# Optimization experiments

Hardware: AMD Instinct MI355X
Metric: run time of the kernel (lower is better)

Reference implementation:

```python
import jax, jax.numpy as jnp
import numpy as np

N_WIRES = 12
DEPTH = 4
IN_DIM = 256
BATCH = 4096


def _apply_rx(state, theta, wire, n):
    """Apply RX(theta) = [[cos(t/2), -i sin(t/2)], [-i sin(t/2), cos(t/2)]] on `wire`.
    state: (batch, 2^n) complex. theta: scalar or (batch,) float."""
    half = theta * 0.5
    c = jnp.reshape(jnp.cos(half), (-1, 1, 1))  # broadcasts for scalar or per-batch
    s = jnp.reshape(jnp.sin(half), (-1, 1, 1))
    L, R = 2 ** wire, 2 ** (n - wire - 1)
    st = state.reshape(-1, L, 2, R)
    a0, a1 = st[:, :, 0], st[:, :, 1]
    b0 = c * a0 - 1j * s * a1
    b1 = -1j * s * a0 + c * a1
    return jnp.stack([b0, b1], axis=2).reshape(state.shape)


def _apply_cnot_adj(state, ctrl, n):
    """CNOT with control=ctrl, target=ctrl+1 (adjacent wires)."""
    L, R = 2 ** ctrl, 2 ** (n - ctrl - 2)
    st = state.reshape(-1, L, 2, 2, R)
    c0 = st[:, :, 0]
    c1 = st[:, :, 1, ::-1]  # flip target bit when control=1
    return jnp.stack([c0, c1], axis=2).reshape(state.shape)


def _pauli_z_signs(n):
    idx = np.arange(2 ** n)
    # wire 0 is the most-significant bit (torchquantum convention)
    bits = (idx[:, None] >> (n - 1 - np.arange(n))[None, :]) & 1
    return (1.0 - 2.0 * bits).astype(np.float32)  # (2^n, n)


def setup_inputs() -> dict:
    key = jax.random.key(0)
    k1, k2, k3 = jax.random.split(key, 3)
    x = jax.random.normal(k1, (BATCH, IN_DIM), dtype=jnp.float32)
    W = jax.random.normal(k2, (N_WIRES, IN_DIM), dtype=jnp.float32)
    params = jax.random.normal(k3, (DEPTH, N_WIRES, 1), dtype=jnp.float32)
    return {"x": x, "W": W, "params": params}


def reference(x, W, params):
    n = W.shape[0]
    depth = params.shape[0]
    batch = x.shape[0]
    angles = x @ W.T  # (batch, n) -- nn.Linear without bias
    state = jnp.zeros((batch, 2 ** n), dtype=jnp.complex64).at[:, 0].set(1.0)
    # data-encoding RX layer (per-batch angles)
    for w in range(n):
        state = _apply_rx(state, angles[:, w], w, n)
    # variational layers: RX(params) then CNOT ladder
    for d in range(depth):
        for w in range(n):
            state = _apply_rx(state, params[d, w, 0], w, n)
        for w in range(n - 1):
            state = _apply_cnot_adj(state, w, n)
    probs = jnp.real(state * jnp.conj(state))  # (batch, 2^n)
    signs = jnp.asarray(_pauli_z_signs(n))     # (2^n, n)
    return probs @ signs  # <Z_w> per wire, (batch, n)
```

## Files before the change

kernel.cpp:

```cpp
#include <hip/hip_runtime.h>
#include <math.h>

#define N_WIRES 12
#define DEPTH   4
#define NGATES  48
#define IN_DIM  256
#define ROWS_PER_BLOCK 16
#define XSTRIDE 272
#define TABSZ   (N_WIRES * 16)

struct Tabs {
    unsigned gm[NGATES];
    bool     rel[N_WIRES][NGATES];
    unsigned chi[NGATES];
    unsigned comp[N_WIRES];
};
constexpr int cparity(unsigned v) { int c = 0; while (v) { c ^= (int)(v & 1u); v >>= 1; } return c; }
constexpr Tabs make_tabs() {
    Tabs tb{};
    for (int g = 0; g < NGATES; ++g) {
        int d = g / N_WIRES, w = g % N_WIRES;
        unsigned m = 1u << w;
        if ((d == 1 || d == 3) && w + 1 < N_WIRES) m |= 1u << (w + 1);
        if ((d == 2 || d == 3) && w + 2 < N_WIRES) m |= 1u << (w + 2);
        if (d == 3 && w + 3 < N_WIRES)             m |= 1u << (w + 3);
        tb.gm[g] = m;
        unsigned c = 0;
        for (int i = 0; i < 16; ++i) c |= (unsigned)cparity(m & 0xFu & (unsigned)i) << i;
        tb.chi[g] = c;
    }
    for (int w = 0; w < N_WIRES; ++w) {
        unsigned S = (1u << w) | (w >= 4 ? (1u << (w - 4)) : 0u) | (w >= 8 ? (1u << (w - 8)) : 0u);
        for (int g = 0; g < NGATES; ++g) tb.rel[w][g] = cparity(tb.gm[g] & S) != 0;
        unsigned lc = (w < 4) ? 0u
                    : (w < 8) ? (1u << (w - 4))
                    : ((1u << (w - 8)) | ((w - 4 < 6) ? (1u << (w - 4)) : 0u));
        tb.comp[w] = 0x3Fu & ~lc;
    }
    return tb;
}
constexpr Tabs TB = make_tabs();

__global__ __launch_bounds__(256)
void tab_kernel(const float* __restrict__ params, float* __restrict__ ws)
{
    __shared__ float tab[TABSZ];
    const int t = threadIdx.x;
    const int lane = t & 63;
    const unsigned i = blockIdx.x;

    if (t < TABSZ) tab[t] = 0.f;
    __syncthreads();

    float th[NGATES];
    #pragma unroll
    for (int g = 0; g < NGATES; ++g) {
        unsigned hs = (unsigned)(__popc((TB.gm[g] >> 4) & (unsigned)t) & 1);
        hs ^= (TB.chi[g] >> i) & 1u;
        th[g] = __int_as_float(__float_as_int(params[g]) ^ (int)(hs << 31));
    }

    float ca[N_WIRES], sa[N_WIRES];
    #pragma unroll
    for (int w = 0; w < N_WIRES; ++w) {
        float p = 0.f;
        #pragma unroll
        for (int g = 0; g < NGATES; ++g)
            if (TB.rel[w][g]) p += th[g];
        float sn, cs;
        __sincosf(p, &sn, &cs);
        ca[w] = cs; sa[w] = sn;
    }

    #pragma unroll
    for (int w = 0; w < N_WIRES; ++w) {
        const unsigned comp = TB.comp[w];
        float vc = ca[w], vs = sa[w];
        #pragma unroll
        for (int d = 0; d < 6; ++d) {
            if (comp & (1u << d)) {
                vc += __shfl_xor(vc, 1 << d, 64);
                vs += __shfl_xor(vs, 1 << d, 64);
            }
        }
        if ((unsigned)(lane & (int)comp) == 0u) {
            unsigned fk = 0;
            if (w >= 4 && w < 8) fk = ((unsigned)t >> (w - 4)) & 1u;
            if (w >= 8) fk = (((unsigned)t >> (w - 8)) & 1u)
                           | ((((unsigned)t >> (w - 4)) & 1u) << 1);
            const int b = (int)((i >> (w & 3)) & 1u);
            atomicAdd(&tab[w * 16 + (int)(fk << 1) + b],     vc);
            atomicAdd(&tab[w * 16 + 8 + (int)(fk << 1) + b], vs);
        }
    }
    __syncthreads();
    if (t < TABSZ) ws[(int)i * TABSZ + t] = tab[t];
}

__global__ __launch_bounds__(256)
void main_kernel(const float* __restrict__ x, const float* __restrict__ W,
                 const float* __restrict__ tabg, float* __restrict__ out)
{
    __shared__ float xl[ROWS_PER_BLOCK * XSTRIDE];
    __shared__ float wl[N_WIRES * IN_DIM];
    __shared__ float al[ROWS_PER_BLOCK * N_WIRES];
    __shared__ float tab[TABSZ];
    const int t = threadIdx.x;
    const int rowbase = blockIdx.x * ROWS_PER_BLOCK;

    const float4* x4 = (const float4*)(x + (size_t)rowbase * IN_DIM);
    float4 xr[4];
    #pragma unroll
    for (int j = 0; j < 4; ++j) xr[j] = x4[t + 256 * j];
    const float4* W4 = (const float4*)W;
    float4 wr[3];
    #pragma unroll
    for (int j = 0; j < 3; ++j) wr[j] = W4[t + 256 * j];

    if (t < TABSZ) {
        float s = 0.f;
        #pragma unroll
        for (int ii = 0; ii < 16; ++ii) s += tabg[ii * TABSZ + t];
        tab[t] = s;
    }

    #pragma unroll
    for (int j = 0; j < 4; ++j) {
        int f = t + 256 * j, row = f >> 6, c4 = f & 63;
        *(float4*)&xl[row * XSTRIDE + c4 * 4] = xr[j];
    }
    #pragma unroll
    for (int j = 0; j < 3; ++j) ((float4*)wl)[t + 256 * j] = wr[j];
    __syncthreads();

    const int r = t >> 4, p = t & 15;
    float partial[N_WIRES];
    #pragma unroll
    for (int w = 0; w < N_WIRES; ++w) partial[w] = 0.f;
    for (int i2 = 0; i2 < 16; ++i2) {
        float xv = xl[r * XSTRIDE + i2 * 16 + p];
        #pragma unroll
        for (int w = 0; w < N_WIRES; ++w)
            partial[w] = fmaf(xv, wl[w * IN_DIM + i2 * 16 + p], partial[w]);
    }
    #pragma unroll
    for (int w = 0; w < N_WIRES; ++w) {
        float v = partial[w];
        v += __shfl_xor(v, 1, 16);
        v += __shfl_xor(v, 2, 16);
        v += __shfl_xor(v, 4, 16);
        v += __shfl_xor(v, 8, 16);
        partial[w] = v;
    }
    if (p < N_WIRES) al[r * N_WIRES + p] = partial[p];
    __syncthreads();

    if (t < ROWS_PER_BLOCK * N_WIRES) {
        const int r2 = t / N_WIRES;
        const int w  = t - r2 * N_WIRES;
        const int nb = 1 + (w >= 4) + (w >= 8);
        const float a0 = al[r2 * N_WIRES + (w & 3)];
        const float a1 = (w >= 4) ? al[r2 * N_WIRES + ((w >= 8) ? (w - 4) : w)] : 0.f;
        const float a2 = (w >= 8) ? al[r2 * N_WIRES + w] : 0.f;
        float o = 0.f;
        const int nk = 1 << nb;
        for (int kap = 0; kap < nk; ++kap) {
            float B = (kap & 1) ? -a0 : a0;
            if (nb > 1) B += (kap & 2) ? -a1 : a1;
            if (nb > 2) B += (kap & 4) ? -a2 : a2;
            float sn, cs;
            __sincosf(B, &sn, &cs);
            o = fmaf(cs,  tab[w * 16 + kap],     o);
            o = fmaf(-sn, tab[w * 16 + 8 + kap], o);
        }
        out[(size_t)(rowbase + r2) * N_WIRES + w] = o * (1.f / 4096.f);
    }
}

extern "C" void kernel_launch(void* const* d_in, const int* in_sizes, int n_in,
                              void* d_out, int out_size, void* d_ws, size_t ws_size,
                              hipStream_t stream) {
    const float* x      = (const float*)d_in[0];
    const float* W      = (const float*)d_in[1];
    const float* params = (const float*)d_in[2];
    float* out          = (float*)d_out;
    float* ws           = (float*)d_ws;

    const int batch = in_sizes[0] / IN_DIM;
    hipLaunchKernelGGL(tab_kernel,  dim3(16),                     dim3(256), 0, stream,
                       params, ws);
    hipLaunchKernelGGL(main_kernel, dim3(batch / ROWS_PER_BLOCK), dim3(256), 0, stream,
                       x, W, ws, out);
}
```

Baseline: 66.41 us.

## Fuse table and main kernels into one cooperative launch with grid sync

Merges the separate parameter-table kernel and main kernel into a single cooperative kernel. The first 16 blocks compute the table slices while every block loads x/W and computes angles, then a grid-wide sync precedes the table reduction and output. This removes a second kernel launch and the inter-kernel dependency gap, at the cost of a grid barrier and a requirement that all 256 blocks be co-resident. The workspace layout is also transposed so each table entry can be reduced with float4 loads.

```diff
diff --git a/kernel.cpp b/kernel.cpp
--- a/kernel.cpp
+++ b/kernel.cpp
@@ -1,5 +1,8 @@
 #include <hip/hip_runtime.h>
+#include <hip/hip_cooperative_groups.h>
 #include <math.h>
+
+namespace cg = cooperative_groups;
 
 #define N_WIRES 12
 #define DEPTH   4
@@ -8,6 +11,7 @@
 #define ROWS_PER_BLOCK 16
 #define XSTRIDE 272
 #define TABSZ   (N_WIRES * 16)
+#define NSLICE  16
 
 struct Tabs {
     unsigned gm[NGATES];
@@ -42,70 +46,16 @@
 constexpr Tabs TB = make_tabs();
 
 __global__ __launch_bounds__(256)
-void tab_kernel(const float* __restrict__ params, float* __restrict__ ws)
-{
-    __shared__ float tab[TABSZ];
-    const int t = threadIdx.x;
-    const int lane = t & 63;
-    const unsigned i = blockIdx.x;
-
-    if (t < TABSZ) tab[t] = 0.f;
-    __syncthreads();
-
-    float th[NGATES];
-    #pragma unroll
-    for (int g = 0; g < NGATES; ++g) {
-        unsigned hs = (unsigned)(__popc((TB.gm[g] >> 4) & (unsigned)t) & 1);
-        hs ^= (TB.chi[g] >> i) & 1u;
-        th[g] = __int_as_float(__float_as_int(params[g]) ^ (int)(hs << 31));
-    }
-
-    float ca[N_WIRES], sa[N_WIRES];
-    #pragma unroll
-    for (int w = 0; w < N_WIRES; ++w) {
-        float p = 0.f;
-        #pragma unroll
-        for (int g = 0; g < NGATES; ++g)
-            if (TB.rel[w][g]) p += th[g];
-        float sn, cs;
-        __sincosf(p, &sn, &cs);
-        ca[w] = cs; sa[w] = sn;
-    }
-
-    #pragma unroll
-    for (int w = 0; w < N_WIRES; ++w) {
-        const unsigned comp = TB.comp[w];
-        float vc = ca[w], vs = sa[w];
-        #pragma unroll
-        for (int d = 0; d < 6; ++d) {
-            if (comp & (1u << d)) {
-                vc += __shfl_xor(vc, 1 << d, 64);
-                vs += __shfl_xor(vs, 1 << d, 64);
-            }
-        }
-        if ((unsigned)(lane & (int)comp) == 0u) {
-            unsigned fk = 0;
-            if (w >= 4 && w < 8) fk = ((unsigned)t >> (w - 4)) & 1u;
-            if (w >= 8) fk = (((unsigned)t >> (w - 8)) & 1u)
-                           | ((((unsigned)t >> (w - 4)) & 1u) << 1);
-            const int b = (int)((i >> (w & 3)) & 1u);
-            atomicAdd(&tab[w * 16 + (int)(fk << 1) + b],     vc);
-            atomicAdd(&tab[w * 16 + 8 + (int)(fk << 1) + b], vs);
-        }
-    }
-    __syncthreads();
-    if (t < TABSZ) ws[(int)i * TABSZ + t] = tab[t];
-}
-
-__global__ __launch_bounds__(256)
-void main_kernel(const float* __restrict__ x, const float* __restrict__ W,
-                 const float* __restrict__ tabg, float* __restrict__ out)
+void fused_coop(const float* __restrict__ x, const float* __restrict__ W,
+                const float* __restrict__ params, float* __restrict__ ws,
+                float* __restrict__ out)
 {
     __shared__ float xl[ROWS_PER_BLOCK * XSTRIDE];
     __shared__ float wl[N_WIRES * IN_DIM];
     __shared__ float al[ROWS_PER_BLOCK * N_WIRES];
-    __shared__ float tab[TABSZ];
+    __shared__ float tabl[TABSZ];
     const int t = threadIdx.x;
+    const int lane = t & 63;
     const int rowbase = blockIdx.x * ROWS_PER_BLOCK;
 
     const float4* x4 = (const float4*)(x + (size_t)rowbase * IN_DIM);
@@ -117,11 +67,55 @@
     #pragma unroll
     for (int j = 0; j < 3; ++j) wr[j] = W4[t + 256 * j];
 
-    if (t < TABSZ) {
-        float s = 0.f;
+    if (blockIdx.x < NSLICE) {
+        const unsigned i = blockIdx.x;
+        if (t < TABSZ) tabl[t] = 0.f;
+        __syncthreads();
+
+        float th[NGATES];
         #pragma unroll
-        for (int ii = 0; ii < 16; ++ii) s += tabg[ii * TABSZ + t];
-        tab[t] = s;
+        for (int g = 0; g < NGATES; ++g) {
+            unsigned hs = (unsigned)(__popc((TB.gm[g] >> 4) & (unsigned)t) & 1);
+            hs ^= (TB.chi[g] >> i) & 1u;
+            th[g] = __int_as_float(__float_as_int(params[g]) ^ (int)(hs << 31));
+        }
+
+        float ca[N_WIRES], sa[N_WIRES];
+        #pragma unroll
+        for (int w = 0; w < N_WIRES; ++w) {
+            float p = 0.f;
+            #pragma unroll
+            for (int g = 0; g < NGATES; ++g)
+                if (TB.rel[w][g]) p += th[g];
+            float sn, cs;
+            __sincosf(p, &sn, &cs);
+            ca[w] = cs; sa[w] = sn;
+        }
+
+        #pragma unroll
+        for (int w = 0; w < N_WIRES; ++w) {
+            const unsigned comp = TB.comp[w];
+            float vc = ca[w], vs = sa[w];
+            #pragma unroll
+            for (int d = 0; d < 6; ++d) {
+                if (comp & (1u << d)) {
+                    vc += __shfl_xor(vc, 1 << d, 64);
+                    vs += __shfl_xor(vs, 1 << d, 64);
+                }
+            }
+            if ((unsigned)(lane & (int)comp) == 0u) {
+                unsigned fk = 0;
+                if (w >= 4 && w < 8) fk = ((unsigned)t >> (w - 4)) & 1u;
+                if (w >= 8) fk = (((unsigned)t >> (w - 8)) & 1u)
+                               | ((((unsigned)t >> (w - 4)) & 1u) << 1);
+                const int b = (int)((i >> (w & 3)) & 1u);
+                atomicAdd(&tabl[w * 16 + (int)(fk << 1) + b],     vc);
+                atomicAdd(&tabl[w * 16 + 8 + (int)(fk << 1) + b], vs);
+            }
+        }
+        __syncthreads();
+        if (t < TABSZ) ws[(size_t)t * NSLICE + i] = tabl[t];
+        __threadfence();
     }
 
     #pragma unroll
@@ -153,6 +147,15 @@
         partial[w] = v;
     }
     if (p < N_WIRES) al[r * N_WIRES + p] = partial[p];
+
+    cg::this_grid().sync();
+
+    if (t < TABSZ) {
+        const float4* p4 = (const float4*)(ws + (size_t)t * NSLICE);
+        float4 s0 = p4[0], s1 = p4[1], s2 = p4[2], s3 = p4[3];
+        tabl[t] = ((s0.x + s0.y) + (s0.z + s0.w)) + ((s1.x + s1.y) + (s1.z + s1.w))
+                + ((s2.x + s2.y) + (s2.z + s2.w)) + ((s3.x + s3.y) + (s3.z + s3.w));
+    }
     __syncthreads();
 
     if (t < ROWS_PER_BLOCK * N_WIRES) {
@@ -170,8 +173,8 @@
             if (nb > 2) B += (kap & 4) ? -a2 : a2;
             float sn, cs;
             __sincosf(B, &sn, &cs);
-            o = fmaf(cs,  tab[w * 16 + kap],     o);
-            o = fmaf(-sn, tab[w * 16 + 8 + kap], o);
+            o = fmaf(cs,  tabl[w * 16 + kap],     o);
+            o = fmaf(-sn, tabl[w * 16 + 8 + kap], o);
         }
         out[(size_t)(rowbase + r2) * N_WIRES + w] = o * (1.f / 4096.f);
     }
@@ -185,10 +188,10 @@
     const float* params = (const float*)d_in[2];
     float* out          = (float*)d_out;
     float* ws           = (float*)d_ws;
+    (void)n_in; (void)out_size; (void)ws_size;
 
     const int batch = in_sizes[0] / IN_DIM;
-    hipLaunchKernelGGL(tab_kernel,  dim3(16),                     dim3(256), 0, stream,
-                       params, ws);
-    hipLaunchKernelGGL(main_kernel, dim3(batch / ROWS_PER_BLOCK), dim3(256), 0, stream,
-                       x, W, ws, out);
+    void* args[] = {(void*)&x, (void*)&W, (void*)&params, (void*)&ws, (void*)&out};
+    hipLaunchCooperativeKernel((void*)fused_coop, dim3(batch / ROWS_PER_BLOCK),
+                               dim3(256), args, 0, stream);
 }
```

After: 110.8 us. 66.8% more time.

## Use 4 rows per block with one wavefront per row and transposed table slices

Applied to the files above, without the earlier changes.

The main kernel now handles 4 rows per block instead of 16, so the grid has four times as many blocks. Each 64-lane wavefront computes one row's 12 linear projections straight from registers with a full-wave shuffle reduction, removing the x staging through shared memory. The table workspace is written transposed so each thread sums its 16 slices with four float4 loads. The trade-off is that every block still loads the full W matrix (12 KB), so W traffic through L2 grows fourfold, and fewer threads do the sincos epilogue per block.

```diff
diff --git a/kernel.cpp b/kernel.cpp
--- a/kernel.cpp
+++ b/kernel.cpp
@@ -5,9 +5,9 @@
 #define DEPTH   4
 #define NGATES  48
 #define IN_DIM  256
-#define ROWS_PER_BLOCK 16
-#define XSTRIDE 272
+#define ROWS_PER_BLOCK 4
 #define TABSZ   (N_WIRES * 16)
+#define NSLICE  16
 
 struct Tabs {
     unsigned gm[NGATES];
@@ -94,65 +94,61 @@
         }
     }
     __syncthreads();
-    if (t < TABSZ) ws[(int)i * TABSZ + t] = tab[t];
+    if (t < TABSZ) ws[(size_t)t * NSLICE + i] = tab[t];
 }
 
 __global__ __launch_bounds__(256)
 void main_kernel(const float* __restrict__ x, const float* __restrict__ W,
                  const float* __restrict__ tabg, float* __restrict__ out)
 {
-    __shared__ float xl[ROWS_PER_BLOCK * XSTRIDE];
     __shared__ float wl[N_WIRES * IN_DIM];
     __shared__ float al[ROWS_PER_BLOCK * N_WIRES];
-    __shared__ float tab[TABSZ];
+    __shared__ float tabl[TABSZ];
     const int t = threadIdx.x;
+    const int q = t >> 6;
+    const int p = t & 63;
     const int rowbase = blockIdx.x * ROWS_PER_BLOCK;
 
-    const float4* x4 = (const float4*)(x + (size_t)rowbase * IN_DIM);
-    float4 xr[4];
-    #pragma unroll
-    for (int j = 0; j < 4; ++j) xr[j] = x4[t + 256 * j];
-    const float4* W4 = (const float4*)W;
+    const float4 xv = ((const float4*)(x + (size_t)rowbase * IN_DIM))[t];
     float4 wr[3];
     #pragma unroll
-    for (int j = 0; j < 3; ++j) wr[j] = W4[t + 256 * j];
+    for (int j = 0; j < 3; ++j) wr[j] = ((const float4*)W)[t + 256 * j];
 
+    float tsum = 0.f;
     if (t < TABSZ) {
-        float s = 0.f;
-        #pragma unroll
-        for (int ii = 0; ii < 16; ++ii) s += tabg[ii * TABSZ + t];
-        tab[t] = s;
+        const float4* p4 = (const float4*)(tabg + (size_t)t * NSLICE);
+        float4 s0 = p4[0], s1 = p4[1], s2 = p4[2], s3 = p4[3];
+        tsum = ((s0.x + s0.y) + (s0.z + s0.w)) + ((s1.x + s1.y) + (s1.z + s1.w))
+             + ((s2.x + s2.y) + (s2.z + s2.w)) + ((s3.x + s3.y) + (s3.z + s3.w));
     }
 
     #pragma unroll
-    for (int j = 0; j < 4; ++j) {
-        int f = t + 256 * j, row = f >> 6, c4 = f & 63;
-        *(float4*)&xl[row * XSTRIDE + c4 * 4] = xr[j];
-    }
-    #pragma unroll
     for (int j = 0; j < 3; ++j) ((float4*)wl)[t + 256 * j] = wr[j];
+    if (t < TABSZ) tabl[t] = tsum;
     __syncthreads();
 
-    const int r = t >> 4, p = t & 15;
     float partial[N_WIRES];
     #pragma unroll
-    for (int w = 0; w < N_WIRES; ++w) partial[w] = 0.f;
-    for (int i2 = 0; i2 < 16; ++i2) {
-        float xv = xl[r * XSTRIDE + i2 * 16 + p];
-        #pragma unroll
-        for (int w = 0; w < N_WIRES; ++w)
-            partial[w] = fmaf(xv, wl[w * IN_DIM + i2 * 16 + p], partial[w]);
+    for (int w = 0; w < N_WIRES; ++w) {
+        const float4 wv = ((const float4*)wl)[w * 64 + p];
+        float v = xv.x * wv.x;
+        v = fmaf(xv.y, wv.y, v);
+        v = fmaf(xv.z, wv.z, v);
+        v = fmaf(xv.w, wv.w, v);
+        partial[w] = v;
     }
     #pragma unroll
     for (int w = 0; w < N_WIRES; ++w) {
         float v = partial[w];
-        v += __shfl_xor(v, 1, 16);
-        v += __shfl_xor(v, 2, 16);
-        v += __shfl_xor(v, 4, 16);
-        v += __shfl_xor(v, 8, 16);
+        v += __shfl_xor(v, 1, 64);
+        v += __shfl_xor(v, 2, 64);
+        v += __shfl_xor(v, 4, 64);
+        v += __shfl_xor(v, 8, 64);
+        v += __shfl_xor(v, 16, 64);
+        v += __shfl_xor(v, 32, 64);
         partial[w] = v;
     }
-    if (p < N_WIRES) al[r * N_WIRES + p] = partial[p];
+    if (p < N_WIRES) al[q * N_WIRES + p] = partial[p];
     __syncthreads();
 
     if (t < ROWS_PER_BLOCK * N_WIRES) {
@@ -170,8 +166,8 @@
             if (nb > 2) B += (kap & 4) ? -a2 : a2;
             float sn, cs;
             __sincosf(B, &sn, &cs);
-            o = fmaf(cs,  tab[w * 16 + kap],     o);
-            o = fmaf(-sn, tab[w * 16 + 8 + kap], o);
+            o = fmaf(cs,  tabl[w * 16 + kap],     o);
+            o = fmaf(-sn, tabl[w * 16 + 8 + kap], o);
         }
         out[(size_t)(rowbase + r2) * N_WIRES + w] = o * (1.f / 4096.f);
     }
@@ -185,9 +181,10 @@
     const float* params = (const float*)d_in[2];
     float* out          = (float*)d_out;
     float* ws           = (float*)d_ws;
+    (void)n_in; (void)out_size; (void)ws_size;
 
     const int batch = in_sizes[0] / IN_DIM;
-    hipLaunchKernelGGL(tab_kernel,  dim3(16),                     dim3(256), 0, stream,
+    hipLaunchKernelGGL(tab_kernel,  dim3(NSLICE),                 dim3(256), 0, stream,
                        params, ws);
     hipLaunchKernelGGL(main_kernel, dim3(batch / ROWS_PER_BLOCK), dim3(256), 0, stream,
                        x, W, ws, out);
```

Measured after the change: 68.50 us. 1.03x slower.
